# Kernel optimization log

Measured on AMD Instinct MI355X. Metric: run time of the kernel, lower is better.

## Reference

```python
import jax, jax.numpy as jnp
import numpy as np

N = 50000   # nodes
E = 400000  # edges
F = 128     # in_channels == heads*out_channels (H*C)
H = 8       # heads
C = 16      # per-head out_channels (hidden_channels)
ED = 16     # edge_dim
G = 64      # num graphs in batch
OUT = 64    # encoder out_channels
NEG = 0.2   # leaky_relu negative slope
EPS = 1e-5  # batchnorm eps


def setup_inputs() -> dict:
    key = jax.random.key(0)
    ks = jax.random.split(key, 16)
    s = 0.09  # ~xavier scale for fan_in 128
    return {
        "x": jax.random.normal(ks[0], (N, F), jnp.float32),
        "edge_index": jax.random.randint(ks[1], (2, E), 0, N, dtype=jnp.int32),
        "edge_attr": jax.random.normal(ks[2], (E, ED), jnp.float32),
        "batch": jnp.sort(jax.random.randint(ks[3], (N,), 0, G, dtype=jnp.int32)),
        "lin_qkv": jax.random.normal(ks[4], (3, 3, F, F), jnp.float32) * s,   # [layer, q/k/v, out, in]
        "lin_edge": jax.random.normal(ks[5], (3, F, ED), jnp.float32) * s,    # [layer, out, edge_dim]
        "att": jax.random.normal(ks[6], (3, 3, H, C), jnp.float32) * 0.1,     # [layer, att_q/att_k/att_edge, H, C]
        "gat_bias": jnp.zeros((3, F), jnp.float32),
        "bn_scale": jnp.ones((3, F), jnp.float32),
        "bn_bias": jnp.zeros((3, F), jnp.float32),
        "W1": jax.random.normal(ks[7], (64, 128), jnp.float32) * s,
        "b1": jnp.zeros((64,), jnp.float32),
        "bn1_s": jnp.ones((64,), jnp.float32),
        "bn1_b": jnp.zeros((64,), jnp.float32),
        "W2": jax.random.normal(ks[8], (32, 64), jnp.float32) * 0.12,
        "b2": jnp.zeros((32,), jnp.float32),
        "bn2_s": jnp.ones((32,), jnp.float32),
        "bn2_b": jnp.zeros((32,), jnp.float32),
        "Wout": jax.random.normal(ks[9], (OUT, 32), jnp.float32) * 0.17,
        "bout": jnp.zeros((OUT,), jnp.float32),
    }


def _bn(h, scale, shift):
    # training-mode BatchNorm1d: biased batch statistics (torch default)
    mu = h.mean(axis=0)
    var = h.var(axis=0)
    return (h - mu) * jax.lax.rsqrt(var + EPS) * scale + shift


def reference(x, edge_index, edge_attr, batch, lin_qkv, lin_edge, att, gat_bias,
              bn_scale, bn_bias, W1, b1, bn1_s, bn1_b, W2, b2, bn2_s, bn2_b, Wout, bout):
    src = edge_index[0]  # j (message source)
    dst = edge_index[1]  # i (message target)
    h = x
    for i in range(3):  # fixed num_layers, structurally distinct params
        q = (h @ lin_qkv[i, 0].T).reshape(N, H, C)
        k = (h @ lin_qkv[i, 1].T).reshape(N, H, C)
        v = (h @ lin_qkv[i, 2].T).reshape(N, H, C)
        e = (edge_attr @ lin_edge[i].T).reshape(E, H, C)
        # alpha = q_i*att_q*(k_j*att_k) + edge*att_edge, summed over C  -> [E,H]
        a = (q[dst] * att[i, 0] * (k[src] * att[i, 1]) + e * att[i, 2]).sum(axis=-1)
        a = jnp.where(a > 0, a, NEG * a)  # leaky_relu
        # segment softmax over incoming edges of each target node
        amax = jax.ops.segment_max(a, dst, num_segments=N)
        a = jnp.exp(a - amax[dst])
        a = a / (jax.ops.segment_sum(a, dst, num_segments=N)[dst] + 1e-16)
        out = jax.ops.segment_sum(v[src] * a[:, :, None], dst, num_segments=N)
        out = out.reshape(N, H * C) + gat_bias[i]  # concat heads + bias
        out = _bn(out, bn_scale[i], bn_bias[i])
        if i < 2:
            out = jax.nn.relu(out)  # dropout p=0.2 inactive in eval
        h = out
    g = jax.ops.segment_max(h, batch, num_segments=G)  # global_max_pool [G, H*C]
    z = jax.nn.relu(_bn(g @ W1.T + b1, bn1_s, bn1_b))
    z = jax.nn.relu(_bn(z @ W2.T + b2, bn2_s, bn2_b))
    return z @ Wout.T + bout  # [G, OUT]
```

## Files before the change

### kernel.cpp

```cpp
#include <hip/hip_runtime.h>
#include <hip/hip_bf16.h>
#include <hip/hip_fp16.h>
#include <cstddef>
#include <cstdint>

#define NN 50000
#define EE 400000
#define GG 64
#define MB 391

typedef __attribute__((ext_vector_type(8))) _Float16 f16x8;
typedef __attribute__((ext_vector_type(4))) float f32x4;

#define GLOAD_LDS16(g, l) __builtin_amdgcn_global_load_lds( \
    (const __attribute__((address_space(1))) void*)(g), \
    (__attribute__((address_space(3))) void*)(l), 16, 0, 0)

__device__ __forceinline__ unsigned f2key(float f) {
    unsigned u = __float_as_uint(f);
    return (u & 0x80000000u) ? ~u : (u | 0x80000000u);
}
__device__ __forceinline__ float key2f(unsigned k) {
    unsigned u = (k & 0x80000000u) ? (k ^ 0x80000000u) : ~k;
    return __uint_as_float(u);
}

__global__ void compute_M_kernel(const float* __restrict__ lin_edge,
                                 const float* __restrict__ att,
                                 float* __restrict__ M) {
    int t = blockIdx.x * 256 + threadIdx.x;
    if (t >= 3 * 128) return;
    int l = t >> 7, r = t & 127, h = r >> 4, d = r & 15;
    const float* le = lin_edge + (size_t)l * 128 * 16;
    const float* av = att + ((l * 3 + 2) * 128) + h * 16;
    float acc = 0.f;
#pragma unroll
    for (int c = 0; c < 16; ++c) acc += le[(h * 16 + c) * 16 + d] * av[c];
    M[t] = acc;
}

__global__ __launch_bounds__(256)
void wpack_kernel(const float* __restrict__ lin_qkv, __half* __restrict__ Wpack) {
    int g = blockIdx.x * 256 + threadIdx.x;
    int lm = g >> 11;
    int r = g & 2047;
    int kb = r >> 9;
    int kg = (r >> 7) & 3;
    int n  = r & 127;
    int k0 = kb * 32 + kg * 8;
    const float* row = lin_qkv + ((size_t)lm * 128 + n) * 128 + k0;
    __half o[8] __attribute__((aligned(16)));
#pragma unroll
    for (int i = 0; i < 8; ++i) o[i] = __float2half(row[i]);
    *reinterpret_cast<uint4*>(Wpack + (size_t)g * 8) = *reinterpret_cast<const uint4*>(o);
}

__global__ __launch_bounds__(256)
void pack_x_kernel(const float* __restrict__ hin, __half* __restrict__ Apack) {
    int s = blockIdx.x * 256 + threadIdx.x;
    int mb = s >> 11;
    int r  = s & 2047;
    int kb = r >> 9;
    int kg = (r >> 7) & 3;
    int m  = r & 127;
    int node = mb * 128 + m;
    int k0 = kb * 32 + kg * 8;
    size_t slot = ((size_t)(mb * 4 + kb) * 512 + (size_t)kg * 128 + m) * 8;
    __half o[8] __attribute__((aligned(16)));
    if (node < NN) {
        const float* row = hin + (size_t)node * 128 + k0;
#pragma unroll
        for (int i = 0; i < 8; ++i) o[i] = __float2half(row[i]);
    } else {
#pragma unroll
        for (int i = 0; i < 8; ++i) o[i] = __float2half(0.f);
    }
    *reinterpret_cast<uint4*>(Apack + slot) = *reinterpret_cast<const uint4*>(o);
}

__global__ __launch_bounds__(256)
void pack_h_kernel(const __half* __restrict__ hin, const float* __restrict__ sums,
                   const float* __restrict__ scale, const float* __restrict__ shift,
                   __half* __restrict__ Apack) {
    int s = blockIdx.x * 256 + threadIdx.x;
    int mb = s >> 11;
    int r  = s & 2047;
    int kb = r >> 9;
    int kg = (r >> 7) & 3;
    int m  = r & 127;
    int node = mb * 128 + m;
    int k0 = kb * 32 + kg * 8;
    size_t slot = ((size_t)(mb * 4 + kb) * 512 + (size_t)kg * 128 + m) * 8;
    __half o[8] __attribute__((aligned(16)));
    if (node < NN) {
        const __half* row = hin + (size_t)node * 128 + k0;
        uint4 raw = *reinterpret_cast<const uint4*>(row);
        const __half* rh = reinterpret_cast<const __half*>(&raw);
#pragma unroll
        for (int i = 0; i < 8; ++i) {
            int c = k0 + i;
            float mu = sums[c] * (1.f / NN);
            float var = sums[128 + c] * (1.f / NN) - mu * mu;
            float v = (__half2float(rh[i]) - mu) * rsqrtf(var + 1e-5f) * scale[c] + shift[c];
            v = v > 0.f ? v : 0.f;
            o[i] = __float2half(v);
        }
    } else {
#pragma unroll
        for (int i = 0; i < 8; ++i) o[i] = __float2half(0.f);
    }
    *reinterpret_cast<uint4*>(Apack + slot) = *reinterpret_cast<const uint4*>(o);
}

__global__ __launch_bounds__(256, 4)
void qkv_mfma_kernel(const __half* __restrict__ Apack,
                     const __half* __restrict__ Wpack,
                     int layer,
                     const float* __restrict__ att_l,
                     __half* __restrict__ qa, __half* __restrict__ kv) {
    __shared__ __half Ab[2][4096];
    __shared__ __half Bb[2][4096];
    const int t = threadIdx.x;
    const int lane = t & 63;
    const int wave = t >> 6;
    const int wr = wave >> 1, wc = wave & 1;
    const int mb = blockIdx.x, mat = blockIdx.y;

    const __half* Abase = Apack + (size_t)mb * 16384;
    const __half* Bbase = Wpack + (size_t)(layer * 3 + mat) * 16384;

    f32x4 acc[4][4];
#pragma unroll
    for (int i = 0; i < 4; ++i)
#pragma unroll
        for (int j = 0; j < 4; ++j) acc[i][j] = (f32x4){0.f, 0.f, 0.f, 0.f};

    auto stage = [&](int c, int buf) {
        const __half* ga = Abase + (size_t)c * 4096;
        const __half* gb = Bbase + (size_t)c * 4096;
        GLOAD_LDS16(ga + (size_t)(wave * 64 + lane) * 8,        &Ab[buf][(wave * 64) * 8]);
        GLOAD_LDS16(ga + (size_t)(256 + wave * 64 + lane) * 8,  &Ab[buf][(256 + wave * 64) * 8]);
        GLOAD_LDS16(gb + (size_t)(wave * 64 + lane) * 8,        &Bb[buf][(wave * 64) * 8]);
        GLOAD_LDS16(gb + (size_t)(256 + wave * 64 + lane) * 8,  &Bb[buf][(256 + wave * 64) * 8]);
    };

    stage(0, 0);
    __syncthreads();
    const int abase = ((lane >> 4) * 128 + wr * 64 + (lane & 15)) * 8;
    const int bbase = ((lane >> 4) * 128 + wc * 64 + (lane & 15)) * 8;
#pragma unroll
    for (int c = 0; c < 4; ++c) {
        int cur = c & 1;
        if (c < 3) stage(c + 1, cur ^ 1);
        f16x8 aF[4], bF[4];
#pragma unroll
        for (int mf = 0; mf < 4; ++mf)
            aF[mf] = *reinterpret_cast<const f16x8*>(&Ab[cur][abase + mf * 128]);
#pragma unroll
        for (int nf = 0; nf < 4; ++nf)
            bF[nf] = *reinterpret_cast<const f16x8*>(&Bb[cur][bbase + nf * 128]);
#pragma unroll
        for (int mf = 0; mf < 4; ++mf)
#pragma unroll
            for (int nf = 0; nf < 4; ++nf)
                acc[mf][nf] = __builtin_amdgcn_mfma_f32_16x16x32_f16(aF[mf], bF[nf], acc[mf][nf], 0, 0, 0);
        __syncthreads();
    }

    __half* outb = (mat == 0) ? qa : kv;
    const size_t stride = (mat == 0) ? 128 : 256;
    const int coloff = (mat == 2) ? 128 : 0;
    float sc[4];
#pragma unroll
    for (int nf = 0; nf < 4; ++nf) {
        int col = wc * 64 + nf * 16 + (lane & 15);
        sc[nf] = (mat == 2) ? 1.f : att_l[mat * 128 + col];
    }
    const int rowq = (lane >> 4) * 4;
#pragma unroll
    for (int mf = 0; mf < 4; ++mf) {
        int row0 = mb * 128 + wr * 64 + mf * 16 + rowq;
#pragma unroll
        for (int reg = 0; reg < 4; ++reg) {
            int row = row0 + reg;
            if (row < NN) {
#pragma unroll
                for (int nf = 0; nf < 4; ++nf) {
                    int col = wc * 64 + nf * 16 + (lane & 15);
                    outb[(size_t)row * stride + coloff + col] = __float2half(acc[mf][nf][reg] * sc[nf]);
                }
            }
        }
    }
}

__global__ __launch_bounds__(256)
void deg_count_kernel(const int* __restrict__ ei, int* __restrict__ deg) {
    int e = blockIdx.x * 256 + threadIdx.x;
    if (e < EE) atomicAdd(&deg[ei[EE + e]], 1);
}

__global__ __launch_bounds__(256)
void scan_partial_kernel(const int* __restrict__ deg, int* __restrict__ psum) {
    __shared__ int red[256];
    int i = blockIdx.x * 256 + threadIdx.x;
    red[threadIdx.x] = (i < NN) ? deg[i] : 0;
    __syncthreads();
    for (int o = 128; o > 0; o >>= 1) {
        if (threadIdx.x < o) red[threadIdx.x] += red[threadIdx.x + o];
        __syncthreads();
    }
    if (threadIdx.x == 0) psum[blockIdx.x] = red[0];
}

__global__ __launch_bounds__(256)
void scan_top_kernel(const int* __restrict__ psum, int* __restrict__ psx) {
    __shared__ int sh[256];
    int t = threadIdx.x;
    int v = (t < 196) ? psum[t] : 0;
    sh[t] = v;
    __syncthreads();
    for (int o = 1; o < 256; o <<= 1) {
        int add = (t >= o) ? sh[t - o] : 0;
        __syncthreads();
        sh[t] += add;
        __syncthreads();
    }
    if (t < 196) psx[t] = sh[t] - v;
}

__global__ __launch_bounds__(256)
void scan_final_kernel(const int* __restrict__ deg, const int* __restrict__ psx,
                       int* __restrict__ offs, int* __restrict__ cursor) {
    __shared__ int sh[256];
    int t = threadIdx.x;
    int i = blockIdx.x * 256 + t;
    int v = (i < NN) ? deg[i] : 0;
    sh[t] = v;
    __syncthreads();
    for (int o = 1; o < 256; o <<= 1) {
        int add = (t >= o) ? sh[t - o] : 0;
        __syncthreads();
        sh[t] += add;
        __syncthreads();
    }
    if (i < NN) {
        int excl = sh[t] - v + psx[blockIdx.x];
        offs[i] = excl;
        cursor[i] = excl;
    }
}

__global__ __launch_bounds__(256)
void scatter_kernel(const int* __restrict__ ei, int* __restrict__ cursor,
                    int2* __restrict__ csr) {
    int e = blockIdx.x * 256 + threadIdx.x;
    if (e < EE) {
        int src = ei[e], dst = ei[EE + e];
        int pos = atomicAdd(&cursor[dst], 1);
        csr[pos] = make_int2(src, e);
    }
}

__global__ __launch_bounds__(256)
void eatt_build_kernel(const float* __restrict__ edge_attr, const int2* __restrict__ csr,
                       const float* __restrict__ M, __half* __restrict__ eatt) {
    __shared__ float Ms[384];
    for (int i = threadIdx.x; i < 384; i += 256) Ms[i] = M[i];
    __syncthreads();
    int pos = blockIdx.x * 256 + threadIdx.x;
    if (pos >= EE) return;
    int e = csr[pos].y;
    const float4* ep = reinterpret_cast<const float4*>(edge_attr + (size_t)e * 16);
    float4 a0 = ep[0], a1 = ep[1], a2 = ep[2], a3 = ep[3];
    float ea[16] = {a0.x, a0.y, a0.z, a0.w, a1.x, a1.y, a1.z, a1.w,
                    a2.x, a2.y, a2.z, a2.w, a3.x, a3.y, a3.z, a3.w};
#pragma unroll
    for (int l = 0; l < 3; ++l) {
        __half o[8] __attribute__((aligned(16)));
#pragma unroll
        for (int h = 0; h < 8; ++h) {
            const float* mp = Ms + l * 128 + h * 16;
            float acc = 0.f;
#pragma unroll
            for (int d = 0; d < 16; ++d) acc += ea[d] * mp[d];
            o[h] = __float2half(acc);
        }
        *reinterpret_cast<uint4*>(eatt + ((size_t)l * EE + pos) * 8) =
            *reinterpret_cast<const uint4*>(o);
    }
}

__global__ __launch_bounds__(128)
void fused_gat_kernel(const __half* __restrict__ qa, const __half* __restrict__ kv,
                      const __half* __restrict__ eatt_l,
                      const int* __restrict__ offs, const int* __restrict__ deg,
                      const int2* __restrict__ csr, __half* __restrict__ hout) {
    int lane = threadIdx.x & 63;
    int n = blockIdx.x * 2 + (threadIdx.x >> 6);
    if (n >= NN) return;
    int h = lane >> 3;
    int c2h = lane & 7;
    int chh = h * 8 + c2h;

    float2 q = __half22float2(reinterpret_cast<const __half2*>(qa + (size_t)n * 128)[chh]);

    int start = offs[n], d = deg[n];
    const __half* ebase = eatt_l + (size_t)start * 8 + h;
    const int2* cbase = csr + start;

    float den = 0.f, acc0 = 0.f, acc1 = 0.f;
    int i = 0;
    for (; i + 8 <= d; i += 8) {
        int s[8]; float e[8]; __half2 kh[8], vh[8];
#pragma unroll
        for (int j = 0; j < 8; ++j) s[j] = cbase[i + j].x;
#pragma unroll
        for (int j = 0; j < 8; ++j) e[j] = __half2float(ebase[(size_t)(i + j) * 8]);
#pragma unroll
        for (int j = 0; j < 8; ++j) {
            const __half2* ph = reinterpret_cast<const __half2*>(kv + (size_t)s[j] * 256);
            kh[j] = ph[chh];
            vh[j] = ph[64 + chh];
        }
#pragma unroll
        for (int j = 0; j < 8; ++j) {
            float2 k = __half22float2(kh[j]);
            float p = q.x * k.x + q.y * k.y;
            p += __shfl_xor(p, 1); p += __shfl_xor(p, 2); p += __shfl_xor(p, 4);
            float a = p + e[j]; a = a > 0.f ? a : 0.2f * a;
            a = fminf(a, 60.f);
            float w = __expf(a);
            float2 v = __half22float2(vh[j]);
            den += w; acc0 += w * v.x; acc1 += w * v.y;
        }
    }
    for (; i + 4 <= d; i += 4) {
        int s[4]; float e[4]; __half2 kh[4], vh[4];
#pragma unroll
        for (int j = 0; j < 4; ++j) s[j] = cbase[i + j].x;
#pragma unroll
        for (int j = 0; j < 4; ++j) e[j] = __half2float(ebase[(size_t)(i + j) * 8]);
#pragma unroll
        for (int j = 0; j < 4; ++j) {
            const __half2* ph = reinterpret_cast<const __half2*>(kv + (size_t)s[j] * 256);
            kh[j] = ph[chh];
            vh[j] = ph[64 + chh];
        }
#pragma unroll
        for (int j = 0; j < 4; ++j) {
            float2 k = __half22float2(kh[j]);
            float p = q.x * k.x + q.y * k.y;
            p += __shfl_xor(p, 1); p += __shfl_xor(p, 2); p += __shfl_xor(p, 4);
            float a = p + e[j]; a = a > 0.f ? a : 0.2f * a;
            a = fminf(a, 60.f);
            float w = __expf(a);
            float2 v = __half22float2(vh[j]);
            den += w; acc0 += w * v.x; acc1 += w * v.y;
        }
    }
    for (; i < d; ++i) {
        int s0 = cbase[i].x;
        float e0 = __half2float(ebase[(size_t)i * 8]);
        const __half2* ph = reinterpret_cast<const __half2*>(kv + (size_t)s0 * 256);
        float2 k = __half22float2(ph[chh]);
        float2 v = __half22float2(ph[64 + chh]);
        float p = q.x * k.x + q.y * k.y;
        p += __shfl_xor(p, 1); p += __shfl_xor(p, 2); p += __shfl_xor(p, 4);
        float a = p + e0; a = a > 0.f ? a : 0.2f * a;
        a = fminf(a, 60.f);
        float w = __expf(a);
        den += w; acc0 += w * v.x; acc1 += w * v.y;
    }
    float inv = 1.f / (den + 1e-16f);
    reinterpret_cast<__half2*>(hout + (size_t)n * 128)[chh] =
        __float22half2_rn(make_float2(acc0 * inv, acc1 * inv));
}

__global__ __launch_bounds__(256)
void bn_stats_kernel(const __half* __restrict__ h, float* __restrict__ sums) {
    __shared__ float red[2][16][128];
    int t = threadIdx.x;
    int cg = t & 15;
    int rofs = t >> 4;
    int r0 = blockIdx.x * 64;
    int rend = min(NN, r0 + 64);
    float s1[8], s2[8];
#pragma unroll
    for (int j = 0; j < 8; ++j) { s1[j] = 0.f; s2[j] = 0.f; }
    for (int r = r0 + rofs; r < rend; r += 16) {
        uint4 raw = *reinterpret_cast<const uint4*>(h + (size_t)r * 128 + cg * 8);
        const __half* rh = reinterpret_cast<const __half*>(&raw);
#pragma unroll
        for (int j = 0; j < 8; ++j) {
            float v = __half2float(rh[j]);
            s1[j] += v; s2[j] += v * v;
        }
    }
#pragma unroll
    for (int j = 0; j < 8; ++j) {
        red[0][rofs][cg * 8 + j] = s1[j];
        red[1][rofs][cg * 8 + j] = s2[j];
    }
    __syncthreads();
    if (t < 128) {
        float a = 0.f, b = 0.f;
#pragma unroll
        for (int i = 0; i < 16; ++i) { a += red[0][i][t]; b += red[1][i][t]; }
        unsafeAtomicAdd(&sums[t], a);
        unsafeAtomicAdd(&sums[128 + t], b);
    }
}

__global__ __launch_bounds__(256)
void bn_pool_kernel(const __half* __restrict__ h, const float* __restrict__ sums,
                    const float* __restrict__ scale, const float* __restrict__ shift,
                    const int* __restrict__ batch, unsigned* __restrict__ gkey) {
    int t = threadIdx.x;
    int c = t & 127, half = t >> 7;
    int r0 = blockIdx.x * 32;
    int rend = min(NN, r0 + 32);
    const float invN = 1.f / (float)NN;
    float mu = sums[c] * invN;
    float var = sums[128 + c] * invN - mu * mu;
    float iscl = rsqrtf(var + 1e-5f) * scale[c];
    float sh = shift[c];
    int curg = -1;
    float lmax = -INFINITY;
    for (int r = r0 + half; r < rend; r += 2) {
        int g = batch[r];
        if (g != curg) {
            if (curg >= 0) atomicMax(&gkey[curg * 128 + c], f2key(lmax));
            curg = g;
            lmax = -INFINITY;
        }
        float v = (__half2float(h[(size_t)r * 128 + c]) - mu) * iscl + sh;
        lmax = fmaxf(lmax, v);
    }
    if (curg >= 0) atomicMax(&gkey[curg * 128 + c], f2key(lmax));
}

__global__ __launch_bounds__(256)
void head_kernel(const unsigned* __restrict__ gkey,
                 const float* __restrict__ W1, const float* __restrict__ b1,
                 const float* __restrict__ bn1s, const float* __restrict__ bn1b,
                 const float* __restrict__ W2, const float* __restrict__ b2,
                 const float* __restrict__ bn2s, const float* __restrict__ bn2b,
                 const float* __restrict__ Wout, const float* __restrict__ bout,
                 float* __restrict__ out) {
    __shared__ float g[64][128];
    __shared__ float z1[64][64];
    __shared__ float z2[64][32];
    int t = threadIdx.x;
    for (int i = t; i < 64 * 128; i += 256) g[i >> 7][i & 127] = key2f(gkey[i]);
    __syncthreads();
    for (int i = t; i < 64 * 64; i += 256) {
        int r = i >> 6, o = i & 63;
        const float* gr = g[r];
        const float* wr = W1 + (size_t)o * 128;
        float acc = b1[o];
        for (int k2 = 0; k2 < 128; ++k2) acc += gr[k2] * wr[k2];
        z1[r][o] = acc;
    }
    __syncthreads();
    if (t < 64) {
        float s1 = 0.f, s2 = 0.f;
        for (int r = 0; r < 64; ++r) { float v = z1[r][t]; s1 += v; s2 += v * v; }
        float mu = s1 * (1.f / 64.f), var = s2 * (1.f / 64.f) - mu * mu;
        float inv = rsqrtf(var + 1e-5f) * bn1s[t];
        float sh = bn1b[t];
        for (int r = 0; r < 64; ++r) {
            float v = (z1[r][t] - mu) * inv + sh;
            z1[r][t] = v > 0.f ? v : 0.f;
        }
    }
    __syncthreads();
    for (int i = t; i < 64 * 32; i += 256) {
        int r = i >> 5, o = i & 31;
        const float* wr = W2 + (size_t)o * 64;
        float acc = b2[o];
        for (int k2 = 0; k2 < 64; ++k2) acc += z1[r][k2] * wr[k2];
        z2[r][o] = acc;
    }
    __syncthreads();
    if (t < 32) {
        float s1 = 0.f, s2 = 0.f;
        for (int r = 0; r < 64; ++r) { float v = z2[r][t]; s1 += v; s2 += v * v; }
        float mu = s1 * (1.f / 64.f), var = s2 * (1.f / 64.f) - mu * mu;
        float inv = rsqrtf(var + 1e-5f) * bn2s[t];
        float sh = bn2b[t];
        for (int r = 0; r < 64; ++r) {
            float v = (z2[r][t] - mu) * inv + sh;
            z2[r][t] = v > 0.f ? v : 0.f;
        }
    }
    __syncthreads();
    for (int i = t; i < 64 * 64; i += 256) {
        int r = i >> 6, o = i & 63;
        const float* wr = Wout + (size_t)o * 32;
        float acc = bout[o];
        for (int k2 = 0; k2 < 32; ++k2) acc += z2[r][k2] * wr[k2];
        out[r * 64 + o] = acc;
    }
}

extern "C" void kernel_launch(void* const* d_in, const int* in_sizes, int n_in,
                              void* d_out, int out_size, void* d_ws, size_t ws_size,
                              hipStream_t stream) {
    const float* x         = (const float*)d_in[0];
    const int*   ei        = (const int*)d_in[1];
    const float* edge_attr = (const float*)d_in[2];
    const int*   batch     = (const int*)d_in[3];
    const float* lin_qkv   = (const float*)d_in[4];
    const float* lin_edge  = (const float*)d_in[5];
    const float* att       = (const float*)d_in[6];
    const float* bn_scale  = (const float*)d_in[8];
    const float* bn_bias   = (const float*)d_in[9];
    const float* W1   = (const float*)d_in[10];
    const float* b1   = (const float*)d_in[11];
    const float* bn1s = (const float*)d_in[12];
    const float* bn1b = (const float*)d_in[13];
    const float* W2   = (const float*)d_in[14];
    const float* b2   = (const float*)d_in[15];
    const float* bn2s = (const float*)d_in[16];
    const float* bn2b = (const float*)d_in[17];
    const float* Wout = (const float*)d_in[18];
    const float* bout = (const float*)d_in[19];

    float* ws = (float*)d_ws;
    size_t off = 0;
    auto alloc = [&](size_t n) { float* p = ws + off; off += n; return p; };
    int*      deg   = (int*)alloc(NN);
    unsigned* gkey  = (unsigned*)alloc(64 * 128);
    float*    gsums = alloc(3 * 256);
    const size_t zeroBytes = ((size_t)NN + 64 * 128 + 3 * 256) * 4;
    __half* hout = (__half*)alloc((size_t)NN * 64);
    __half* qa   = (__half*)alloc((size_t)NN * 64);
    __half* kv   = (__half*)alloc((size_t)NN * 128);
    __half* Apack = (__half*)alloc((size_t)MB * 8192);
    __half* Wpack = (__half*)alloc(9 * 8192);
    int*    offs   = (int*)alloc(NN);
    int*    cursor = (int*)alloc(NN);
    int2*   csr    = (int2*)alloc((size_t)EE * 2);
    __half* eatt   = (__half*)alloc((size_t)3 * EE * 4);
    int*    psum   = (int*)alloc(256);
    int*    psx    = (int*)alloc(256);
    float*  M      = alloc(3 * 128);

    const int edgeBlocks = (EE + 255) / 256;
    const int scanBlocks = (NN + 255) / 256;
    const int packBlocks = MB * 8;
    const int statBlocks = (NN + 63) / 64;
    const int poolBlocks = (NN + 31) / 32;
    const int gatBlocks  = (NN + 1) / 2;

    hipMemsetAsync(deg, 0, zeroBytes, stream);
    wpack_kernel<<<72, 256, 0, stream>>>(lin_qkv, Wpack);
    compute_M_kernel<<<2, 256, 0, stream>>>(lin_edge, att, M);
    deg_count_kernel<<<edgeBlocks, 256, 0, stream>>>(ei, deg);
    scan_partial_kernel<<<scanBlocks, 256, 0, stream>>>(deg, psum);
    scan_top_kernel<<<1, 256, 0, stream>>>(psum, psx);
    scan_final_kernel<<<scanBlocks, 256, 0, stream>>>(deg, psx, offs, cursor);
    scatter_kernel<<<edgeBlocks, 256, 0, stream>>>(ei, cursor, csr);
    eatt_build_kernel<<<edgeBlocks, 256, 0, stream>>>(edge_attr, csr, M, eatt);
    pack_x_kernel<<<packBlocks, 256, 0, stream>>>(x, Apack);

    for (int l = 0; l < 3; ++l) {
        qkv_mfma_kernel<<<dim3(MB, 3), 256, 0, stream>>>(
            Apack, Wpack, l, att + (size_t)l * 384, qa, kv);

        fused_gat_kernel<<<gatBlocks, 128, 0, stream>>>(
            qa, kv, eatt + (size_t)l * EE * 8, offs, deg, csr, hout);

        bn_stats_kernel<<<statBlocks, 256, 0, stream>>>(hout, gsums + l * 256);

        if (l < 2) {
            pack_h_kernel<<<packBlocks, 256, 0, stream>>>(
                hout, gsums + l * 256, bn_scale + l * 128, bn_bias + l * 128, Apack);
        } else {
            bn_pool_kernel<<<poolBlocks, 256, 0, stream>>>(
                hout, gsums + l * 256, bn_scale + l * 128, bn_bias + l * 128, batch, gkey);
        }
    }

    head_kernel<<<1, 256, 0, stream>>>(gkey, W1, b1, bn1s, bn1b, W2, b2, bn2s, bn2b, Wout, bout, (float*)d_out);
}
```

Baseline: 393.5 us.

## Restructure QKV GEMM to 64-row tiles computing all three matrices per block

```diff
diff --git a/kernel.cpp b/kernel.cpp
--- a/kernel.cpp
+++ b/kernel.cpp
@@ -8,6 +8,7 @@
 #define EE 400000
 #define GG 64
 #define MB 391
+#define MB2 782
 
 typedef __attribute__((ext_vector_type(8))) _Float16 f16x8;
 typedef __attribute__((ext_vector_type(4))) float f32x4;
@@ -118,76 +119,86 @@
                      int layer,
                      const float* __restrict__ att_l,
                      __half* __restrict__ qa, __half* __restrict__ kv) {
-    __shared__ __half Ab[2][4096];
+    __shared__ __half As[4][2048];
     __shared__ __half Bb[2][4096];
     const int t = threadIdx.x;
     const int lane = t & 63;
     const int wave = t >> 6;
     const int wr = wave >> 1, wc = wave & 1;
-    const int mb = blockIdx.x, mat = blockIdx.y;
-
-    const __half* Abase = Apack + (size_t)mb * 16384;
-    const __half* Bbase = Wpack + (size_t)(layer * 3 + mat) * 16384;
-
-    f32x4 acc[4][4];
-#pragma unroll
-    for (int i = 0; i < 4; ++i)
-#pragma unroll
-        for (int j = 0; j < 4; ++j) acc[i][j] = (f32x4){0.f, 0.f, 0.f, 0.f};
-
-    auto stage = [&](int c, int buf) {
-        const __half* ga = Abase + (size_t)c * 4096;
-        const __half* gb = Bbase + (size_t)c * 4096;
-        GLOAD_LDS16(ga + (size_t)(wave * 64 + lane) * 8,        &Ab[buf][(wave * 64) * 8]);
-        GLOAD_LDS16(ga + (size_t)(256 + wave * 64 + lane) * 8,  &Ab[buf][(256 + wave * 64) * 8]);
-        GLOAD_LDS16(gb + (size_t)(wave * 64 + lane) * 8,        &Bb[buf][(wave * 64) * 8]);
-        GLOAD_LDS16(gb + (size_t)(256 + wave * 64 + lane) * 8,  &Bb[buf][(256 + wave * 64) * 8]);
-    };
-
-    stage(0, 0);
-    __syncthreads();
-    const int abase = ((lane >> 4) * 128 + wr * 64 + (lane & 15)) * 8;
+    const int r0 = blockIdx.x * 64;
+    const int mbk = blockIdx.x >> 1;
+    const int half = blockIdx.x & 1;
+
+    const __half* Abase = Apack + (size_t)mbk * 16384;
+    const __half* Bl = Wpack + (size_t)layer * 3 * 16384;
+
+#pragma unroll
+    for (int kb = 0; kb < 4; ++kb) {
+        const __half* ga = Abase + (size_t)kb * 4096 + (size_t)(t >> 6) * 1024 + half * 512 + (size_t)(t & 63) * 8;
+        GLOAD_LDS16(ga, &As[kb][((t >> 6) * 64 + (t & 63)) * 8]);
+    }
+    {
+        const __half* gb = Bl + (size_t)t * 8;
+        GLOAD_LDS16(gb, &Bb[0][(size_t)t * 8]);
+        GLOAD_LDS16(gb + 2048, &Bb[0][2048 + (size_t)t * 8]);
+    }
+    __syncthreads();
+
+    const int abase = ((lane >> 4) * 64 + wr * 32 + (lane & 15)) * 8;
     const int bbase = ((lane >> 4) * 128 + wc * 64 + (lane & 15)) * 8;
-#pragma unroll
-    for (int c = 0; c < 4; ++c) {
-        int cur = c & 1;
-        if (c < 3) stage(c + 1, cur ^ 1);
-        f16x8 aF[4], bF[4];
-#pragma unroll
-        for (int mf = 0; mf < 4; ++mf)
-            aF[mf] = *reinterpret_cast<const f16x8*>(&Ab[cur][abase + mf * 128]);
-#pragma unroll
-        for (int nf = 0; nf < 4; ++nf)
-            bF[nf] = *reinterpret_cast<const f16x8*>(&Bb[cur][bbase + nf * 128]);
-#pragma unroll
-        for (int mf = 0; mf < 4; ++mf)
+    const int rowq = (lane >> 4) * 4;
+
+    for (int mat = 0; mat < 3; ++mat) {
+        f32x4 acc[2][4];
+#pragma unroll
+        for (int i = 0; i < 2; ++i)
+#pragma unroll
+            for (int j = 0; j < 4; ++j) acc[i][j] = (f32x4){0.f, 0.f, 0.f, 0.f};
+
+#pragma unroll
+        for (int c = 0; c < 4; ++c) {
+            int g = mat * 4 + c;
+            if (g < 11) {
+                const __half* gb = Bl + (size_t)(g + 1) * 4096 + (size_t)t * 8;
+                GLOAD_LDS16(gb, &Bb[(g + 1) & 1][(size_t)t * 8]);
+                GLOAD_LDS16(gb + 2048, &Bb[(g + 1) & 1][2048 + (size_t)t * 8]);
+            }
+            f16x8 aF[2], bF[4];
+#pragma unroll
+            for (int mf = 0; mf < 2; ++mf)
+                aF[mf] = *reinterpret_cast<const f16x8*>(&As[c][abase + mf * 128]);
 #pragma unroll
             for (int nf = 0; nf < 4; ++nf)
-                acc[mf][nf] = __builtin_amdgcn_mfma_f32_16x16x32_f16(aF[mf], bF[nf], acc[mf][nf], 0, 0, 0);
-        __syncthreads();
-    }
-
-    __half* outb = (mat == 0) ? qa : kv;
-    const size_t stride = (mat == 0) ? 128 : 256;
-    const int coloff = (mat == 2) ? 128 : 0;
-    float sc[4];
-#pragma unroll
-    for (int nf = 0; nf < 4; ++nf) {
-        int col = wc * 64 + nf * 16 + (lane & 15);
-        sc[nf] = (mat == 2) ? 1.f : att_l[mat * 128 + col];
-    }
-    const int rowq = (lane >> 4) * 4;
-#pragma unroll
-    for (int mf = 0; mf < 4; ++mf) {
-        int row0 = mb * 128 + wr * 64 + mf * 16 + rowq;
-#pragma unroll
-        for (int reg = 0; reg < 4; ++reg) {
-            int row = row0 + reg;
-            if (row < NN) {
-#pragma unroll
-                for (int nf = 0; nf < 4; ++nf) {
-                    int col = wc * 64 + nf * 16 + (lane & 15);
-                    outb[(size_t)row * stride + coloff + col] = __float2half(acc[mf][nf][reg] * sc[nf]);
+                bF[nf] = *reinterpret_cast<const f16x8*>(&Bb[g & 1][bbase + nf * 128]);
+#pragma unroll
+            for (int mf = 0; mf < 2; ++mf)
+#pragma unroll
+                for (int nf = 0; nf < 4; ++nf)
+                    acc[mf][nf] = __builtin_amdgcn_mfma_f32_16x16x32_f16(aF[mf], bF[nf], acc[mf][nf], 0, 0, 0);
+            __syncthreads();
+        }
+
+        __half* outb = (mat == 0) ? qa : kv;
+        const size_t stride = (mat == 0) ? 128 : 256;
+        const int coloff = (mat == 2) ? 128 : 0;
+        float sc[4];
+#pragma unroll
+        for (int nf = 0; nf < 4; ++nf) {
+            int col = wc * 64 + nf * 16 + (lane & 15);
+            sc[nf] = (mat == 2) ? 1.f : att_l[mat * 128 + col];
+        }
+#pragma unroll
+        for (int mf = 0; mf < 2; ++mf) {
+            int row0 = r0 + wr * 32 + mf * 16 + rowq;
+#pragma unroll
+            for (int reg = 0; reg < 4; ++reg) {
+                int row = row0 + reg;
+                if (row < NN) {
+#pragma unroll
+                    for (int nf = 0; nf < 4; ++nf) {
+                        int col = wc * 64 + nf * 16 + (lane & 15);
+                        outb[(size_t)row * stride + coloff + col] = __float2half(acc[mf][nf][reg] * sc[nf]);
+                    }
                 }
             }
         }
@@ -566,7 +577,7 @@
     pack_x_kernel<<<packBlocks, 256, 0, stream>>>(x, Apack);
 
     for (int l = 0; l < 3; ++l) {
-        qkv_mfma_kernel<<<dim3(MB, 3), 256, 0, stream>>>(
+        qkv_mfma_kernel<<<MB2, 256, 0, stream>>>(
             Apack, Wpack, l, att + (size_t)l * 384, qa, kv);
 
         fused_gat_kernel<<<gatBlocks, 128, 0, stream>>>(
```

Result: no change. 387.0 us (-1.7%).
